# Kernel optimization log

Measured on AMD Instinct MI355X. Metric: run time of the kernel, lower is better.

Reference implementation:

```python
import jax, jax.numpy as jnp
import numpy as np

B, S, D = 8, 2048, 512
KD = 64          # key_dim == value_dim
WIDTH = 128      # attention_width
NEG = 1.0e9


def setup_inputs() -> dict:
    key = jax.random.key(0)
    ks = jax.random.split(key, 16)
    glorot_dd = float(np.sqrt(6.0 / (D + KD)))
    glorot_sd = float(np.sqrt(6.0 / (S + KD)))
    u = lambda k, shape, lim: jax.random.uniform(k, shape, jnp.float32, -lim, lim)
    return {
        "x": jax.random.normal(ks[0], (B, S, D), jnp.float32),
        "Wqr": u(ks[1], (D, KD), glorot_dd), "bqr": jnp.zeros((KD,), jnp.float32),
        "Wqi": u(ks[2], (D, KD), glorot_dd), "bqi": jnp.zeros((KD,), jnp.float32),
        "Wkr": u(ks[3], (D, KD), glorot_dd), "bkr": jnp.zeros((KD,), jnp.float32),
        "Wki": u(ks[4], (D, KD), glorot_dd), "bki": jnp.zeros((KD,), jnp.float32),
        "Wv": u(ks[5], (D, KD), glorot_dd),  "bv": jnp.zeros((KD,), jnp.float32),
        "pos_qr": u(ks[6], (S, KD), glorot_sd), "pos_qi": u(ks[7], (S, KD), glorot_sd),
        "pos_kr": u(ks[8], (S, KD), glorot_sd), "pos_ki": u(ks[9], (S, KD), glorot_sd),
        "temperature": jnp.ones((1,), jnp.float32),
    }


def _masks():
    ind = jnp.arange(S)
    band = (jnp.abs(ind[:, None] - ind[None, :]) <= WIDTH).astype(jnp.float32)  # [S,S]
    causal = jnp.tril(jnp.ones((S, S), jnp.float32))                            # [S,S]
    return band, causal


def reference(x, Wqr, bqr, Wqi, bqi, Wkr, bkr, Wki, bki, Wv, bv,
              pos_qr, pos_qi, pos_kr, pos_ki, temperature):
    scale = 1.0 / jnp.sqrt(jnp.float32(KD))
    # complex Q/K via two real Dense layers; Q scaled BEFORE adding interference
    qr = (x @ Wqr + bqr) * scale + pos_qr[None]   # [B,S,KD]
    qi = (x @ Wqi + bqi) * scale + pos_qi[None]
    kr = (x @ Wkr + bkr) + pos_kr[None]
    ki = (x @ Wki + bki) + pos_ki[None]
    v = x @ Wv + bv                                # [B,S,KD]
    # real part of complex Q @ K^T (transpose, not conjugate-transpose)
    scores = (jnp.einsum('bsd,btd->bst', qr, kr)
              - jnp.einsum('bsd,btd->bst', qi, ki)) * scale  # [B,S,S]
    band, causal = _masks()
    scores = scores * band - NEG * (1.0 - band)
    scores = scores * causal - NEG * (1.0 - causal)
    probs = jax.nn.softmax(scores * temperature[0], axis=-1)
    return jnp.einsum('bst,btd->bsd', probs, v)
```

## Files before the change

kernel.cpp:

```cpp
#include <hip/hip_runtime.h>

#define NB 8
#define NS 2048
#define ND 512
#define NKD 64
#define NM (NB*NS)

typedef _Float16 f16x8 __attribute__((ext_vector_type(8)));
typedef float f32x4 __attribute__((ext_vector_type(4)));


__global__ __launch_bounds__(256) void wprep_kernel(
    const float* __restrict__ w0, const float* __restrict__ w1,
    const float* __restrict__ w2, const float* __restrict__ w3,
    const float* __restrict__ w4,
    f16x8* __restrict__ wfrag)
{
    const int t = blockIdx.x * 256 + threadIdx.x;
    const int p    = t >> 12;
    const int nf   = (t >> 10) & 3;
    const int kt   = (t >> 6) & 15;
    const int lane = t & 63;
    const float* __restrict__ W = (p==0)?w0:(p==1)?w1:(p==2)?w2:(p==3)?w3:w4;
    const int n  = nf*16 + (lane & 15);
    const int k0 = kt*32 + (lane >> 4)*8;
    f16x8 v;
    #pragma unroll
    for (int j = 0; j < 8; ++j)
        v[j] = (_Float16)W[(size_t)(k0 + j)*NKD + n];
    wfrag[t] = v;
}

__global__ __launch_bounds__(256) void proj_mfma(
    const float* __restrict__ x,
    const f16x8* __restrict__ wfrag,
    const float* __restrict__ b0, const float* __restrict__ b1,
    const float* __restrict__ b2, const float* __restrict__ b3,
    const float* __restrict__ b4,
    const float* __restrict__ p0, const float* __restrict__ p1,
    const float* __restrict__ p2, const float* __restrict__ p3,
    _Float16* __restrict__ qkri,
    _Float16* __restrict__ vT)
{
    const int g    = (blockIdx.x * 256 + threadIdx.x) >> 6;
    const int lane = threadIdx.x & 63;
    const int m0   = g * 16;

    const int row = m0 + (lane & 15);
    const int kb  = (lane >> 4) * 8;
    const float* __restrict__ xrow = x + (size_t)row * ND + kb;
    const f16x8* __restrict__ wf   = wfrag + lane;

    f32x4 acc[5][4];
    #pragma unroll
    for (int p = 0; p < 5; ++p)
        #pragma unroll
        for (int nf = 0; nf < 4; ++nf) acc[p][nf] = (f32x4){0.f,0.f,0.f,0.f};

    for (int kt = 0; kt < 16; ++kt) {
        float4 xa = *(const float4*)(xrow + kt*32);
        float4 xb = *(const float4*)(xrow + kt*32 + 4);
        f16x8 a;
        a[0]=(_Float16)xa.x; a[1]=(_Float16)xa.y;
        a[2]=(_Float16)xa.z; a[3]=(_Float16)xa.w;
        a[4]=(_Float16)xb.x; a[5]=(_Float16)xb.y;
        a[6]=(_Float16)xb.z; a[7]=(_Float16)xb.w;
        #pragma unroll
        for (int p = 0; p < 5; ++p)
            #pragma unroll
            for (int nf = 0; nf < 4; ++nf) {
                f16x8 b = wf[(p*4 + nf)*1024 + kt*64];
                acc[p][nf] = __builtin_amdgcn_mfma_f32_16x16x32_f16(a, b, acc[p][nf], 0, 0, 0);
            }
    }

    const float* biases[5] = {b0, b1, b2, b3, b4};
    const float* poss[4]   = {p0, p1, p2, p3};

    const int col   = lane & 15;
    const int rbase = (lane >> 4) << 2;
    const int bidx  = m0 >> 11;

    #pragma unroll
    for (int p = 0; p < 4; ++p) {
        _Float16* ob = qkri + ((size_t)p*NM + m0) * NKD;
        #pragma unroll
        for (int nf = 0; nf < 4; ++nf) {
            const int c = nf*16 + col;
            const float bb = biases[p][c];
            #pragma unroll
            for (int r = 0; r < 4; ++r) {
                const int mm = rbase + r;
                const int s  = (m0 + mm) & (NS - 1);
                float t = acc[p][nf][r] + bb;
                if (p < 2) t = t * 0.125f + poss[p][s*NKD + c];
                else       t = t + poss[p][s*NKD + c];
                ob[(size_t)mm*NKD + c] = (_Float16)t;
            }
        }
    }
    {
        _Float16* vb = vT + (size_t)bidx*NKD*NS;
        #pragma unroll
        for (int nf = 0; nf < 4; ++nf) {
            const int c = nf*16 + col;
            const float bb = b4[c];
            #pragma unroll
            for (int r = 0; r < 4; ++r) {
                const int s = (m0 + rbase + r) & (NS - 1);
                vb[(size_t)c*NS + s] = (_Float16)(acc[4][nf][r] + bb);
            }
        }
    }
}

#define QB 64
#define NT 12
#define KITEMS (NT*2*64)
#define PSTR 200
#define ATTN_LDS (3*NT*2*64*16 + 4*16*PSTR*2)

__global__ __launch_bounds__(256) void attn_mfma(
    const _Float16* __restrict__ qkri,
    const _Float16* __restrict__ vT,
    const float* __restrict__ temp,
    float* __restrict__ out)
{
    extern __shared__ __align__(16) char smem[];
    _Float16* krf = (_Float16*)smem;
    _Float16* kif = krf + KITEMS*8;
    _Float16* vf  = kif + KITEMS*8;
    _Float16* pl  = vf  + 6*4*64*8;

    const int tid  = threadIdx.x;
    const int w    = tid >> 6;
    const int lane = tid & 63;
    const int i0   = blockIdx.x * QB;
    const int b    = blockIdx.y;
    const int jb   = i0 - 128;

    const _Float16* __restrict__ qr_g = qkri + ((size_t)0*NM + (size_t)b*NS)*NKD;
    const _Float16* __restrict__ qi_g = qkri + ((size_t)1*NM + (size_t)b*NS)*NKD;
    const _Float16* __restrict__ kr_g = qkri + ((size_t)2*NM + (size_t)b*NS)*NKD;
    const _Float16* __restrict__ ki_g = qkri + ((size_t)3*NM + (size_t)b*NS)*NKD;
    const _Float16* __restrict__ vT_b = vT + (size_t)b*NKD*NS;

    for (int it = tid; it < 2*KITEMS; it += 256) {
        const int mtx = (it >= KITEMS) ? 1 : 0;
        const int r   = it - mtx*KITEMS;
        const int t   = r >> 7;
        const int kt  = (r >> 6) & 1;
        const int ln  = r & 63;
        const int row = jb + 16*t + (ln & 15);
        const int d0  = kt*32 + (ln >> 4)*8;
        f16x8 v = {};
        if (row >= 0)
            v = *(const f16x8*)&(mtx ? ki_g : kr_g)[(size_t)row*NKD + d0];
        ((f16x8*)(mtx ? kif : krf))[r] = v;
    }
    for (int it = tid; it < 6*4*64; it += 256) {
        const int kt = it >> 8;
        const int nf = (it >> 6) & 3;
        const int ln = it & 63;
        const int d  = nf*16 + (ln & 15);
        const int k0 = jb + kt*32 + (ln >> 4)*8;
        f16x8 v = {};
        if (k0 >= 0)
            v = *(const f16x8*)&vT_b[(size_t)d*NS + k0];
        ((f16x8*)vf)[it] = v;
    }

    const int qrow = i0 + 16*w + (lane & 15);
    const int d0   = (lane >> 4)*8;
    f16x8 aqr[2], aqi[2];
    #pragma unroll
    for (int kt = 0; kt < 2; ++kt) {
        aqr[kt] = *(const f16x8*)&qr_g[(size_t)qrow*NKD + kt*32 + d0];
        f16x8 qi8 = *(const f16x8*)&qi_g[(size_t)qrow*NKD + kt*32 + d0];
        aqi[kt] = -qi8;
    }
    __syncthreads();

    f32x4 st[9];
    #pragma unroll
    for (int t = 0; t < 9; ++t) {
        const int tt = w + t;
        f32x4 acc = (f32x4){0.f,0.f,0.f,0.f};
        acc = __builtin_amdgcn_mfma_f32_16x16x32_f16(aqr[0], ((f16x8*)krf)[(tt*2+0)*64+lane], acc, 0,0,0);
        acc = __builtin_amdgcn_mfma_f32_16x16x32_f16(aqr[1], ((f16x8*)krf)[(tt*2+1)*64+lane], acc, 0,0,0);
        acc = __builtin_amdgcn_mfma_f32_16x16x32_f16(aqi[0], ((f16x8*)kif)[(tt*2+0)*64+lane], acc, 0,0,0);
        acc = __builtin_amdgcn_mfma_f32_16x16x32_f16(aqi[1], ((f16x8*)kif)[(tt*2+1)*64+lane], acc, 0,0,0);
        st[t] = acc;
    }

    const float sT  = 0.125f * temp[0];
    const int col   = lane & 15;
    const int qg4   = (lane >> 4) * 4;
    const int jrmin = -jb;
    float mx[4] = {-3e38f, -3e38f, -3e38f, -3e38f};
    #pragma unroll
    for (int t = 0; t < 9; ++t) {
        const int jr = 16*(w + t) + col;
        #pragma unroll
        for (int r = 0; r < 4; ++r) {
            const int row16 = 16*w + qg4 + r;
            const bool ok = (jr >= row16) && (jr <= 128 + row16) && (jr >= jrmin);
            const float s = ok ? st[t][r]*sT : -1e30f;
            st[t][r] = s;
            mx[r] = fmaxf(mx[r], s);
        }
    }
    #pragma unroll
    for (int off = 1; off < 16; off <<= 1)
        #pragma unroll
        for (int r = 0; r < 4; ++r)
            mx[r] = fmaxf(mx[r], __shfl_xor(mx[r], off, 16));

    float sum[4] = {0.f, 0.f, 0.f, 0.f};
    #pragma unroll
    for (int t = 0; t < 9; ++t)
        #pragma unroll
        for (int r = 0; r < 4; ++r) {
            const float e = __expf(st[t][r] - mx[r]);
            st[t][r] = e;
            sum[r] += e;
        }
    #pragma unroll
    for (int off = 1; off < 16; off <<= 1)
        #pragma unroll
        for (int r = 0; r < 4; ++r)
            sum[r] += __shfl_xor(sum[r], off, 16);
    float inv[4];
    #pragma unroll
    for (int r = 0; r < 4; ++r) inv[r] = 1.0f / sum[r];

    _Float16* plw = pl + w*16*PSTR;
    #pragma unroll
    for (int t = 0; t < 9; ++t) {
        const int jr = 16*(w + t) + col;
        #pragma unroll
        for (int r = 0; r < 4; ++r)
            plw[(qg4 + r)*PSTR + jr] = (_Float16)(st[t][r] * inv[r]);
    }
    {
        const int tz = (w & 1) ? (w - 1) : (w + 9);
        #pragma unroll
        for (int r = 0; r < 4; ++r)
            plw[(qg4 + r)*PSTR + 16*tz + col] = (_Float16)0.f;
    }
    __syncthreads();

    f32x4 oacc[4];
    #pragma unroll
    for (int nf = 0; nf < 4; ++nf) oacc[nf] = (f32x4){0.f,0.f,0.f,0.f};
    const int ktlo = w >> 1;
    const _Float16* pa = plw + (lane & 15)*PSTR + (lane >> 4)*8;
    #pragma unroll
    for (int kk = 0; kk < 5; ++kk) {
        const int kt = ktlo + kk;
        f16x8 a = *(const f16x8*)(pa + kt*32);
        #pragma unroll
        for (int nf = 0; nf < 4; ++nf)
            oacc[nf] = __builtin_amdgcn_mfma_f32_16x16x32_f16(
                a, ((f16x8*)vf)[(kt*4+nf)*64+lane], oacc[nf], 0,0,0);
    }

    float* ob = out + ((size_t)b*NS + i0 + 16*w)*NKD;
    #pragma unroll
    for (int nf = 0; nf < 4; ++nf)
        #pragma unroll
        for (int r = 0; r < 4; ++r)
            ob[(size_t)(qg4 + r)*NKD + nf*16 + col] = oacc[nf][r];
}

extern "C" void kernel_launch(void* const* d_in, const int* in_sizes, int n_in,
                              void* d_out, int out_size, void* d_ws, size_t ws_size,
                              hipStream_t stream)
{
    const float* x    = (const float*)d_in[0];
    const float* w0   = (const float*)d_in[1];
    const float* b0   = (const float*)d_in[2];
    const float* w1   = (const float*)d_in[3];
    const float* b1   = (const float*)d_in[4];
    const float* w2   = (const float*)d_in[5];
    const float* b2   = (const float*)d_in[6];
    const float* w3   = (const float*)d_in[7];
    const float* b3   = (const float*)d_in[8];
    const float* w4   = (const float*)d_in[9];
    const float* b4   = (const float*)d_in[10];
    const float* p0   = (const float*)d_in[11];
    const float* p1   = (const float*)d_in[12];
    const float* p2   = (const float*)d_in[13];
    const float* p3   = (const float*)d_in[14];
    const float* temp = (const float*)d_in[15];

    char* ws = (char*)d_ws;
    f16x8*    wfrag = (f16x8*)ws;
    _Float16* qkri  = (_Float16*)(ws + 327680);
    _Float16* vT    = (_Float16*)(ws + 327680 + 8388608);

    wprep_kernel<<<80, 256, 0, stream>>>(w0, w1, w2, w3, w4, wfrag);

    proj_mfma<<<256, 256, 0, stream>>>(x, wfrag,
                                       b0, b1, b2, b3, b4,
                                       p0, p1, p2, p3, qkri, vT);

    hipFuncSetAttribute((const void*)attn_mfma,
                        hipFuncAttributeMaxDynamicSharedMemorySize, ATTN_LDS);
    dim3 gB(NS/QB, NB);
    attn_mfma<<<gB, 256, ATTN_LDS, stream>>>(qkri, vT, temp, (float*)d_out);
}
```

Baseline: 42.30 us.

## Use one-wave attention blocks loading K/V fragments directly from global memory

Shrinks the attention block from four waves over 64 queries to a single wave over 16 queries, and drops the shared-memory staging of K and V. Each wave now loads its K and V MFMA operands straight from global memory and keeps only the probability tile in LDS. This removes the cooperative staging loop and its barrier and raises the number of independent blocks. The cost is that overlapping K/V windows are re-read by neighbouring blocks through L2 instead of being shared within a block, and the direct loads are strided.

```diff
diff --git a/kernel.cpp b/kernel.cpp
--- a/kernel.cpp
+++ b/kernel.cpp
@@ -114,28 +114,18 @@
     }
 }
 
-#define QB 64
-#define NT 12
-#define KITEMS (NT*2*64)
 #define PSTR 200
-#define ATTN_LDS (3*NT*2*64*16 + 4*16*PSTR*2)
-
-__global__ __launch_bounds__(256) void attn_mfma(
+
+__global__ __launch_bounds__(64) void attn_mfma(
     const _Float16* __restrict__ qkri,
     const _Float16* __restrict__ vT,
     const float* __restrict__ temp,
     float* __restrict__ out)
 {
-    extern __shared__ __align__(16) char smem[];
-    _Float16* krf = (_Float16*)smem;
-    _Float16* kif = krf + KITEMS*8;
-    _Float16* vf  = kif + KITEMS*8;
-    _Float16* pl  = vf  + 6*4*64*8;
-
-    const int tid  = threadIdx.x;
-    const int w    = tid >> 6;
-    const int lane = tid & 63;
-    const int i0   = blockIdx.x * QB;
+    __shared__ _Float16 pl[16 * PSTR];
+
+    const int lane = threadIdx.x;
+    const int i0   = blockIdx.x * 16;
     const int b    = blockIdx.y;
     const int jb   = i0 - 128;
 
@@ -145,33 +135,8 @@
     const _Float16* __restrict__ ki_g = qkri + ((size_t)3*NM + (size_t)b*NS)*NKD;
     const _Float16* __restrict__ vT_b = vT + (size_t)b*NKD*NS;
 
-    for (int it = tid; it < 2*KITEMS; it += 256) {
-        const int mtx = (it >= KITEMS) ? 1 : 0;
-        const int r   = it - mtx*KITEMS;
-        const int t   = r >> 7;
-        const int kt  = (r >> 6) & 1;
-        const int ln  = r & 63;
-        const int row = jb + 16*t + (ln & 15);
-        const int d0  = kt*32 + (ln >> 4)*8;
-        f16x8 v = {};
-        if (row >= 0)
-            v = *(const f16x8*)&(mtx ? ki_g : kr_g)[(size_t)row*NKD + d0];
-        ((f16x8*)(mtx ? kif : krf))[r] = v;
-    }
-    for (int it = tid; it < 6*4*64; it += 256) {
-        const int kt = it >> 8;
-        const int nf = (it >> 6) & 3;
-        const int ln = it & 63;
-        const int d  = nf*16 + (ln & 15);
-        const int k0 = jb + kt*32 + (ln >> 4)*8;
-        f16x8 v = {};
-        if (k0 >= 0)
-            v = *(const f16x8*)&vT_b[(size_t)d*NS + k0];
-        ((f16x8*)vf)[it] = v;
-    }
-
-    const int qrow = i0 + 16*w + (lane & 15);
-    const int d0   = (lane >> 4)*8;
+    const int qrow = i0 + (lane & 15);
+    const int d0   = (lane >> 4) * 8;
     f16x8 aqr[2], aqi[2];
     #pragma unroll
     for (int kt = 0; kt < 2; ++kt) {
@@ -179,17 +144,24 @@
         f16x8 qi8 = *(const f16x8*)&qi_g[(size_t)qrow*NKD + kt*32 + d0];
         aqi[kt] = -qi8;
     }
-    __syncthreads();
-
+
+    const f16x8 zf = {};
     f32x4 st[9];
     #pragma unroll
     for (int t = 0; t < 9; ++t) {
-        const int tt = w + t;
+        const int row = jb + 16*t + (lane & 15);
+        const bool ok = (row >= 0);
+        const _Float16* krp = kr_g + (size_t)row*NKD + d0;
+        const _Float16* kip = ki_g + (size_t)row*NKD + d0;
+        f16x8 bkr0 = ok ? *(const f16x8*)(krp)      : zf;
+        f16x8 bkr1 = ok ? *(const f16x8*)(krp + 32) : zf;
+        f16x8 bki0 = ok ? *(const f16x8*)(kip)      : zf;
+        f16x8 bki1 = ok ? *(const f16x8*)(kip + 32) : zf;
         f32x4 acc = (f32x4){0.f,0.f,0.f,0.f};
-        acc = __builtin_amdgcn_mfma_f32_16x16x32_f16(aqr[0], ((f16x8*)krf)[(tt*2+0)*64+lane], acc, 0,0,0);
-        acc = __builtin_amdgcn_mfma_f32_16x16x32_f16(aqr[1], ((f16x8*)krf)[(tt*2+1)*64+lane], acc, 0,0,0);
-        acc = __builtin_amdgcn_mfma_f32_16x16x32_f16(aqi[0], ((f16x8*)kif)[(tt*2+0)*64+lane], acc, 0,0,0);
-        acc = __builtin_amdgcn_mfma_f32_16x16x32_f16(aqi[1], ((f16x8*)kif)[(tt*2+1)*64+lane], acc, 0,0,0);
+        acc = __builtin_amdgcn_mfma_f32_16x16x32_f16(aqr[0], bkr0, acc, 0,0,0);
+        acc = __builtin_amdgcn_mfma_f32_16x16x32_f16(aqr[1], bkr1, acc, 0,0,0);
+        acc = __builtin_amdgcn_mfma_f32_16x16x32_f16(aqi[0], bki0, acc, 0,0,0);
+        acc = __builtin_amdgcn_mfma_f32_16x16x32_f16(aqi[1], bki1, acc, 0,0,0);
         st[t] = acc;
     }
 
@@ -200,10 +172,10 @@
     float mx[4] = {-3e38f, -3e38f, -3e38f, -3e38f};
     #pragma unroll
     for (int t = 0; t < 9; ++t) {
-        const int jr = 16*(w + t) + col;
+        const int jr = 16*t + col;
         #pragma unroll
         for (int r = 0; r < 4; ++r) {
-            const int row16 = 16*w + qg4 + r;
+            const int row16 = qg4 + r;
             const bool ok = (jr >= row16) && (jr <= 128 + row16) && (jr >= jrmin);
             const float s = ok ? st[t][r]*sT : -1e30f;
             st[t][r] = s;
@@ -234,38 +206,36 @@
     #pragma unroll
     for (int r = 0; r < 4; ++r) inv[r] = 1.0f / sum[r];
 
-    _Float16* plw = pl + w*16*PSTR;
     #pragma unroll
     for (int t = 0; t < 9; ++t) {
-        const int jr = 16*(w + t) + col;
-        #pragma unroll
-        for (int r = 0; r < 4; ++r)
-            plw[(qg4 + r)*PSTR + jr] = (_Float16)(st[t][r] * inv[r]);
-    }
-    {
-        const int tz = (w & 1) ? (w - 1) : (w + 9);
-        #pragma unroll
-        for (int r = 0; r < 4; ++r)
-            plw[(qg4 + r)*PSTR + 16*tz + col] = (_Float16)0.f;
-    }
+        const int jr = 16*t + col;
+        #pragma unroll
+        for (int r = 0; r < 4; ++r)
+            pl[(qg4 + r)*PSTR + jr] = (_Float16)(st[t][r] * inv[r]);
+    }
+    #pragma unroll
+    for (int r = 0; r < 4; ++r)
+        pl[(qg4 + r)*PSTR + 144 + col] = (_Float16)0.f;
     __syncthreads();
 
     f32x4 oacc[4];
     #pragma unroll
     for (int nf = 0; nf < 4; ++nf) oacc[nf] = (f32x4){0.f,0.f,0.f,0.f};
-    const int ktlo = w >> 1;
-    const _Float16* pa = plw + (lane & 15)*PSTR + (lane >> 4)*8;
-    #pragma unroll
-    for (int kk = 0; kk < 5; ++kk) {
-        const int kt = ktlo + kk;
+    const _Float16* pa = pl + (lane & 15)*PSTR + (lane >> 4)*8;
+    #pragma unroll
+    for (int kt = 0; kt < 5; ++kt) {
         f16x8 a = *(const f16x8*)(pa + kt*32);
-        #pragma unroll
-        for (int nf = 0; nf < 4; ++nf)
-            oacc[nf] = __builtin_amdgcn_mfma_f32_16x16x32_f16(
-                a, ((f16x8*)vf)[(kt*4+nf)*64+lane], oacc[nf], 0,0,0);
-    }
-
-    float* ob = out + ((size_t)b*NS + i0 + 16*w)*NKD;
+        const int k0 = jb + kt*32 + (lane >> 4)*8;
+        const bool okv = (k0 >= 0);
+        #pragma unroll
+        for (int nf = 0; nf < 4; ++nf) {
+            const int d = nf*16 + (lane & 15);
+            f16x8 bv = okv ? *(const f16x8*)&vT_b[(size_t)d*NS + k0] : zf;
+            oacc[nf] = __builtin_amdgcn_mfma_f32_16x16x32_f16(a, bv, oacc[nf], 0,0,0);
+        }
+    }
+
+    float* ob = out + ((size_t)b*NS + i0)*NKD;
     #pragma unroll
     for (int nf = 0; nf < 4; ++nf)
         #pragma unroll
@@ -305,8 +275,6 @@
                                        b0, b1, b2, b3, b4,
                                        p0, p1, p2, p3, qkri, vT);
 
-    hipFuncSetAttribute((const void*)attn_mfma,
-                        hipFuncAttributeMaxDynamicSharedMemorySize, ATTN_LDS);
-    dim3 gB(NS/QB, NB);
-    attn_mfma<<<gB, 256, ATTN_LDS, stream>>>(qkri, vT, temp, (float*)d_out);
-}
+    dim3 gB(NS/16, NB);
+    attn_mfma<<<gB, 64, 0, stream>>>(qkri, vT, temp, (float*)d_out);
+}
```

After: 46.71 us. 1.1x slower.
